# Performance work log

Measured on AMD Instinct MI355X. Metric: run time of the kernel, lower is better.

The kernel has to match this reference:

```python
import jax, jax.numpy as jnp
import numpy as np

N = 67108864  # 2**26 bytes per stream


def brev(x):
    """Reverse the 8 bits of each uint8 byte (same math as torch brev helper)."""
    x = x.astype(jnp.uint32)
    x = ((x & 0x55) << 1) | ((x >> 1) & 0x55)
    x = ((x & 0x33) << 2) | ((x >> 2) & 0x33)
    x = ((x & 0x0F) << 4) | ((x >> 4) & 0x0F)
    return x.astype(jnp.uint8)


def setup_inputs() -> dict:
    key = jax.random.key(0)
    k1, k2 = jax.random.split(key)
    a = jax.random.randint(k1, (N,), 0, 256, dtype=jnp.int32).astype(jnp.uint8)
    b = jax.random.randint(k2, (N,), 0, 256, dtype=jnp.int32).astype(jnp.uint8)
    return {"a": a, "b": b}


def _bs_add(a, b):
    """Bit-serial carry-propagate add: brev -> wrapping add -> global carry
    resolution via exclusive scan (cub_exclusive_scan equivalent) -> brev."""
    ar = brev(a)
    br = brev(b)
    c = ar + br                                   # uint8 wrapping add
    g = (c < ar).astype(jnp.uint8)                # carry generated (wrapped)
    p = (c == 255).astype(jnp.uint8)              # carry propagates (max)

    def op(l, r):
        gl, pl = l
        gr, pr = r
        return (gr | (pr & gl), pl & pr)

    gi, _ = jax.lax.associative_scan(op, (g.ravel(), p.ravel()))
    # exclusive scan: incoming carry for element i is carry-out of prefix [0, i)
    carry_in = jnp.concatenate([jnp.zeros((1,), jnp.uint8), gi[:-1]]).reshape(c.shape)
    res = (c + carry_in).astype(jnp.uint8)        # resolve carries (wrapping)
    return brev(res)


def reference(a, b):
    m_plus_c = _bs_add(a, b)          # BSAdd
    not_c = ~b                        # BSNot on original b
    return m_plus_c & not_c           # BSAnd
```

## Files before the change

### kernel.cpp

```cpp
#include <hip/hip_runtime.h>


#define BLK 256
#define EPT 16
#define WTILE (64 * EPT)

typedef int iv4 __attribute__((ext_vector_type(4)));

__device__ __forceinline__ unsigned brev8(unsigned x) {
    return __brev(x) >> 24;
}

__global__ __launch_bounds__(BLK) void bss_wave(const int* __restrict__ a,
                                                const int* __restrict__ b,
                                                int* __restrict__ out) {
    const int tid = threadIdx.x;
    const int lane = tid & 63;
    const int wid = tid >> 6;
    const long gw = (long)blockIdx.x * (BLK / 64) + wid;
    const long base0 = gw * WTILE;
    const int base = (int)base0 + lane * EPT;

    iv4 av[4], bv[4];
#pragma unroll
    for (int q = 0; q < 4; ++q) {
        av[q] = *reinterpret_cast<const iv4*>(a + base + q * 4);
        bv[q] = *reinterpret_cast<const iv4*>(b + base + q * 4);
    }
    const int* ae = reinterpret_cast<const int*>(av);
    const int* be = reinterpret_cast<const int*>(bv);

    unsigned cb = 0u;
    {
        long w = base0 - 64;
        for (;;) {
            long idx = w + lane;
            unsigned cc = 0u, gg = 0u;
            if (idx >= 0) {
                unsigned s = brev8((unsigned)a[idx]) + brev8((unsigned)b[idx]);
                cc = s & 0xFFu;
                gg = s >> 8;
            }
            unsigned long long m = __ballot(cc != 0xFFu);
            if (m) {
                int hi = 63 - __clzll(m);
                cb = (unsigned)__shfl((int)gg, hi, 64);
                break;
            }
            w -= 64;
        }
    }

    unsigned c[EPT];
    unsigned G = 0u, P = 0u;
#pragma unroll
    for (int k = 0; k < EPT; ++k) {
        unsigned s = brev8((unsigned)ae[k]) + brev8((unsigned)be[k]);
        c[k] = s & 0xFFu;
        G |= (s >> 8) << k;
        P |= ((c[k] + 1u) >> 8) << k;
    }

    const unsigned GoP = G | P;
    const unsigned g_t = (G + GoP) >> EPT;
    const unsigned p_t = (P == 0xFFFFu) ? 1u : 0u;

    const unsigned long long Gw = __ballot(g_t != 0u);
    const unsigned long long Pw = __ballot(p_t != 0u);
    const unsigned long long Sw = Gw + (Gw | Pw) + (unsigned long long)cb;
    const unsigned c_t = (unsigned)(((Pw ^ Sw) >> lane) & 1ull);

    const unsigned Cm = P ^ (G + GoP + c_t);

    iv4 o[4];
    int* of = reinterpret_cast<int*>(o);
#pragma unroll
    for (int k = 0; k < EPT; ++k) {
        unsigned res = (c[k] + ((Cm >> k) & 1u)) & 0xFFu;
        of[k] = (int)(brev8(res) & (~(unsigned)be[k] & 0xFFu));
    }
#pragma unroll
    for (int q = 0; q < 4; ++q)
        *reinterpret_cast<iv4*>(out + base + q * 4) = o[q];
}

extern "C" void kernel_launch(void* const* d_in, const int* in_sizes, int n_in,
                              void* d_out, int out_size, void* d_ws, size_t ws_size,
                              hipStream_t stream) {
    const int* a = (const int*)d_in[0];
    const int* b = (const int*)d_in[1];
    int* out = (int*)d_out;
    const int n = in_sizes[0];
    const int nblk = n / (WTILE * (BLK / 64));

    bss_wave<<<nblk, BLK, 0, stream>>>(a, b, out);
}
```

Measured before the change: 152.2 us.

## Process four sub-tiles per wave with double-buffered loads and chained carry

Each wave now handles four consecutive 1024-element sub-tiles. It carries the wave-level carry-out from one sub-tile into the next, so the backward lookback scan only runs once per four sub-tiles. Loads for the next sub-tile are issued before computing the current one, overlapping memory latency with compute. The trade-offs are higher register pressure, a quarter as many blocks (less parallelism), and a serial dependency chain within each wave.

```diff
diff --git a/kernel.cpp b/kernel.cpp
--- a/kernel.cpp
+++ b/kernel.cpp
@@ -3,12 +3,63 @@
 
 #define BLK 256
 #define EPT 16
-#define WTILE (64 * EPT)
+#define WSUB (64 * EPT)
+#define KSUB 4
+#define WSPAN (WSUB * KSUB)
+#define WAVES (BLK / 64)
 
 typedef int iv4 __attribute__((ext_vector_type(4)));
 
 __device__ __forceinline__ unsigned brev8(unsigned x) {
     return __brev(x) >> 24;
+}
+
+__device__ __forceinline__ void load_sub(const int* __restrict__ a,
+                                         const int* __restrict__ b,
+                                         int base, iv4* av, iv4* bv) {
+#pragma unroll
+    for (int q = 0; q < 4; ++q) {
+        av[q] = *reinterpret_cast<const iv4*>(a + base + q * 4);
+        bv[q] = *reinterpret_cast<const iv4*>(b + base + q * 4);
+    }
+}
+
+__device__ __forceinline__ unsigned comp_sub(const iv4* av, const iv4* bv,
+                                             int base, int lane, unsigned cb,
+                                             int* __restrict__ out) {
+    const int* ae = reinterpret_cast<const int*>(av);
+    const int* be = reinterpret_cast<const int*>(bv);
+    unsigned c[EPT], G = 0u, P = 0u;
+#pragma unroll
+    for (int k = 0; k < EPT; ++k) {
+        unsigned s = brev8((unsigned)ae[k]) + brev8((unsigned)be[k]);
+        c[k] = s & 0xFFu;
+        G |= (s >> 8) << k;
+        P |= ((c[k] + 1u) >> 8) << k;
+    }
+    const unsigned GoP = G | P;
+    const unsigned g_t = (G + GoP) >> EPT;
+    const unsigned p_t = (P == 0xFFFFu) ? 1u : 0u;
+
+    const unsigned long long Gw = __ballot(g_t != 0u);
+    const unsigned long long Pw = __ballot(p_t != 0u);
+    const unsigned long long T  = Gw + (Gw | Pw);
+    const unsigned long long Sw = T + (unsigned long long)cb;
+    const unsigned cout = (unsigned)((T < Gw) | (Sw < T));
+    const unsigned c_t  = (unsigned)(((Pw ^ Sw) >> lane) & 1ull);
+    const unsigned Cm = P ^ (G + GoP + c_t);
+
+    iv4 o[4];
+    int* of = reinterpret_cast<int*>(o);
+#pragma unroll
+    for (int k = 0; k < EPT; ++k) {
+        unsigned res = (c[k] + ((Cm >> k) & 1u)) & 0xFFu;
+        of[k] = (int)(brev8(res) & (~(unsigned)be[k] & 0xFFu));
+    }
+#pragma unroll
+    for (int q = 0; q < 4; ++q)
+        *reinterpret_cast<iv4*>(out + base + q * 4) = o[q];
+    return cout;
 }
 
 __global__ __launch_bounds__(BLK) void bss_wave(const int* __restrict__ a,
@@ -17,22 +68,16 @@
     const int tid = threadIdx.x;
     const int lane = tid & 63;
     const int wid = tid >> 6;
-    const long gw = (long)blockIdx.x * (BLK / 64) + wid;
-    const long base0 = gw * WTILE;
-    const int base = (int)base0 + lane * EPT;
+    const long w0 = ((long)blockIdx.x * WAVES + wid) * WSPAN;
+    const int sb = (int)w0 + lane * EPT;
 
-    iv4 av[4], bv[4];
-#pragma unroll
-    for (int q = 0; q < 4; ++q) {
-        av[q] = *reinterpret_cast<const iv4*>(a + base + q * 4);
-        bv[q] = *reinterpret_cast<const iv4*>(b + base + q * 4);
-    }
-    const int* ae = reinterpret_cast<const int*>(av);
-    const int* be = reinterpret_cast<const int*>(bv);
+    iv4 avA[4], bvA[4], avB[4], bvB[4];
+    load_sub(a, b, sb,        avA, bvA);
+    load_sub(a, b, sb + WSUB, avB, bvB);
 
     unsigned cb = 0u;
     {
-        long w = base0 - 64;
+        long w = w0 - 64;
         for (;;) {
             long idx = w + lane;
             unsigned cc = 0u, gg = 0u;
@@ -51,37 +96,12 @@
         }
     }
 
-    unsigned c[EPT];
-    unsigned G = 0u, P = 0u;
-#pragma unroll
-    for (int k = 0; k < EPT; ++k) {
-        unsigned s = brev8((unsigned)ae[k]) + brev8((unsigned)be[k]);
-        c[k] = s & 0xFFu;
-        G |= (s >> 8) << k;
-        P |= ((c[k] + 1u) >> 8) << k;
-    }
-
-    const unsigned GoP = G | P;
-    const unsigned g_t = (G + GoP) >> EPT;
-    const unsigned p_t = (P == 0xFFFFu) ? 1u : 0u;
-
-    const unsigned long long Gw = __ballot(g_t != 0u);
-    const unsigned long long Pw = __ballot(p_t != 0u);
-    const unsigned long long Sw = Gw + (Gw | Pw) + (unsigned long long)cb;
-    const unsigned c_t = (unsigned)(((Pw ^ Sw) >> lane) & 1ull);
-
-    const unsigned Cm = P ^ (G + GoP + c_t);
-
-    iv4 o[4];
-    int* of = reinterpret_cast<int*>(o);
-#pragma unroll
-    for (int k = 0; k < EPT; ++k) {
-        unsigned res = (c[k] + ((Cm >> k) & 1u)) & 0xFFu;
-        of[k] = (int)(brev8(res) & (~(unsigned)be[k] & 0xFFu));
-    }
-#pragma unroll
-    for (int q = 0; q < 4; ++q)
-        *reinterpret_cast<iv4*>(out + base + q * 4) = o[q];
+    cb = comp_sub(avA, bvA, sb,            lane, cb, out);
+    load_sub(a, b, sb + 2 * WSUB, avA, bvA);
+    cb = comp_sub(avB, bvB, sb + WSUB,     lane, cb, out);
+    load_sub(a, b, sb + 3 * WSUB, avB, bvB);
+    cb = comp_sub(avA, bvA, sb + 2 * WSUB, lane, cb, out);
+    (void)comp_sub(avB, bvB, sb + 3 * WSUB, lane, cb, out);
 }
 
 extern "C" void kernel_launch(void* const* d_in, const int* in_sizes, int n_in,
@@ -91,7 +111,7 @@
     const int* b = (const int*)d_in[1];
     int* out = (int*)d_out;
     const int n = in_sizes[0];
-    const int nblk = n / (WTILE * (BLK / 64));
+    const int nblk = n / (WSPAN * WAVES);
 
     bss_wave<<<nblk, BLK, 0, stream>>>(a, b, out);
 }
```

Result: slower. 161.9 us (+6.4%).

## Coalesce wave loads into contiguous 256-element chunks with chained carry

Applied to the files above, without the earlier changes.

Each lane now handles 4 contiguous elements in each of 4 chunks, so a whole wave reads a contiguous 1 KB chunk per load instead of each lane striding over 16 elements. The wave-level carry scan runs once per chunk, and the carry-out of each 64-bit ballot add is chained into the next chunk. This is meant to improve memory coalescing, at the cost of four ballot/scan rounds per wave instead of one.

```diff
diff --git a/kernel.cpp b/kernel.cpp
--- a/kernel.cpp
+++ b/kernel.cpp
@@ -2,8 +2,10 @@
 
 
 #define BLK 256
-#define EPT 16
-#define WTILE (64 * EPT)
+#define CHUNK 256
+#define NCHUNK 4
+#define WTILE (CHUNK * NCHUNK)
+#define WAVES (BLK / 64)
 
 typedef int iv4 __attribute__((ext_vector_type(4)));
 
@@ -11,28 +13,25 @@
     return __brev(x) >> 24;
 }
 
-__global__ __launch_bounds__(BLK) void bss_wave(const int* __restrict__ a,
+__global__ __launch_bounds__(BLK) void bss_coal(const int* __restrict__ a,
                                                 const int* __restrict__ b,
                                                 int* __restrict__ out) {
     const int tid = threadIdx.x;
     const int lane = tid & 63;
     const int wid = tid >> 6;
-    const long gw = (long)blockIdx.x * (BLK / 64) + wid;
-    const long base0 = gw * WTILE;
-    const int base = (int)base0 + lane * EPT;
+    const long w0 = ((long)blockIdx.x * WAVES + wid) * WTILE;
 
-    iv4 av[4], bv[4];
+    iv4 av[NCHUNK], bv[NCHUNK];
 #pragma unroll
-    for (int q = 0; q < 4; ++q) {
-        av[q] = *reinterpret_cast<const iv4*>(a + base + q * 4);
-        bv[q] = *reinterpret_cast<const iv4*>(b + base + q * 4);
+    for (int q = 0; q < NCHUNK; ++q) {
+        const int off = (int)w0 + q * CHUNK + lane * 4;
+        av[q] = *reinterpret_cast<const iv4*>(a + off);
+        bv[q] = *reinterpret_cast<const iv4*>(b + off);
     }
-    const int* ae = reinterpret_cast<const int*>(av);
-    const int* be = reinterpret_cast<const int*>(bv);
 
     unsigned cb = 0u;
     {
-        long w = base0 - 64;
+        long w = w0 - 64;
         for (;;) {
             long idx = w + lane;
             unsigned cc = 0u, gg = 0u;
@@ -51,37 +50,37 @@
         }
     }
 
-    unsigned c[EPT];
-    unsigned G = 0u, P = 0u;
 #pragma unroll
-    for (int k = 0; k < EPT; ++k) {
-        unsigned s = brev8((unsigned)ae[k]) + brev8((unsigned)be[k]);
-        c[k] = s & 0xFFu;
-        G |= (s >> 8) << k;
-        P |= ((c[k] + 1u) >> 8) << k;
+    for (int q = 0; q < NCHUNK; ++q) {
+        unsigned c[4], G = 0u, P = 0u;
+#pragma unroll
+        for (int j = 0; j < 4; ++j) {
+            unsigned s = brev8((unsigned)av[q][j]) + brev8((unsigned)bv[q][j]);
+            c[j] = s & 0xFFu;
+            G |= (s >> 8) << j;
+            P |= ((c[j] + 1u) >> 8) << j;
+        }
+        const unsigned GoP = G | P;
+        const unsigned g_t = (G + GoP) >> 4;
+        const unsigned p_t = (P == 0xFu) ? 1u : 0u;
+
+        const unsigned long long Gw = __ballot(g_t != 0u);
+        const unsigned long long Pw = __ballot(p_t != 0u);
+        const unsigned long long T  = Gw + (Gw | Pw);
+        const unsigned long long Sw = T + (unsigned long long)cb;
+        const unsigned cout = (unsigned)((T < Gw) | (Sw < T));
+        const unsigned c_t  = (unsigned)(((Pw ^ Sw) >> lane) & 1ull);
+        const unsigned Cm = P ^ (G + GoP + c_t);
+
+        iv4 o;
+#pragma unroll
+        for (int j = 0; j < 4; ++j) {
+            unsigned res = (c[j] + ((Cm >> j) & 1u)) & 0xFFu;
+            o[j] = (int)(brev8(res) & (~(unsigned)bv[q][j] & 0xFFu));
+        }
+        *reinterpret_cast<iv4*>(out + (int)w0 + q * CHUNK + lane * 4) = o;
+        cb = cout;
     }
-
-    const unsigned GoP = G | P;
-    const unsigned g_t = (G + GoP) >> EPT;
-    const unsigned p_t = (P == 0xFFFFu) ? 1u : 0u;
-
-    const unsigned long long Gw = __ballot(g_t != 0u);
-    const unsigned long long Pw = __ballot(p_t != 0u);
-    const unsigned long long Sw = Gw + (Gw | Pw) + (unsigned long long)cb;
-    const unsigned c_t = (unsigned)(((Pw ^ Sw) >> lane) & 1ull);
-
-    const unsigned Cm = P ^ (G + GoP + c_t);
-
-    iv4 o[4];
-    int* of = reinterpret_cast<int*>(o);
-#pragma unroll
-    for (int k = 0; k < EPT; ++k) {
-        unsigned res = (c[k] + ((Cm >> k) & 1u)) & 0xFFu;
-        of[k] = (int)(brev8(res) & (~(unsigned)be[k] & 0xFFu));
-    }
-#pragma unroll
-    for (int q = 0; q < 4; ++q)
-        *reinterpret_cast<iv4*>(out + base + q * 4) = o[q];
 }
 
 extern "C" void kernel_launch(void* const* d_in, const int* in_sizes, int n_in,
@@ -91,7 +90,7 @@
     const int* b = (const int*)d_in[1];
     int* out = (int*)d_out;
     const int n = in_sizes[0];
-    const int nblk = n / (WTILE * (BLK / 64));
+    const int nblk = n / (WTILE * WAVES);
 
-    bss_wave<<<nblk, BLK, 0, stream>>>(a, b, out);
+    bss_coal<<<nblk, BLK, 0, stream>>>(a, b, out);
 }
```

New measurement: 144.6 us (median of 2 runs). -5.0%, faster.
